# Kernel optimization log

Hardware: AMD Instinct MI355X
Metric: run time of the kernel (lower is better)

Reference implementation:

```python
import jax, jax.numpy as jnp
import numpy as np

D_MODEL, D_STATE, D_CONV, D_INNER, DT_RANK, K = 96, 16, 3, 192, 6, 4
B, H, W = 1, 64, 64


def setup_inputs() -> dict:
    key = jax.random.key(0)
    ks = jax.random.split(key, 10)
    x = jax.random.normal(ks[0], (B, H, W, D_MODEL), jnp.float32)
    in_proj_w = jax.random.normal(ks[1], (2 * D_INNER, D_MODEL), jnp.float32) * 0.02
    conv_w = jax.random.normal(ks[2], (D_INNER, 1, D_CONV, D_CONV), jnp.float32) * 0.1
    conv_b = jnp.zeros((D_INNER,), jnp.float32)
    x_proj_w = jax.random.normal(ks[3], (K, DT_RANK + 2 * D_STATE, D_INNER), jnp.float32) * 0.02
    dt_std = DT_RANK ** -0.5
    dt_w = jax.random.uniform(ks[4], (K, D_INNER, DT_RANK), jnp.float32, -dt_std, dt_std)
    # dt bias init: inv-softplus of dt ~ logUniform(1e-3, 1e-1)
    u = jax.random.uniform(ks[5], (K, D_INNER), jnp.float32)
    dt = jnp.exp(u * (np.log(0.1) - np.log(0.001)) + np.log(0.001)).clip(1e-4)
    dt_b = dt + jnp.log(-jnp.expm1(-dt))
    A_logs = jnp.log(jnp.broadcast_to(jnp.arange(1, D_STATE + 1, dtype=jnp.float32), (K * D_INNER, D_STATE)))
    Ds = jnp.ones((K * D_INNER,), jnp.float32)
    ln_g = jnp.ones((D_INNER,), jnp.float32)
    ln_b = jnp.zeros((D_INNER,), jnp.float32)
    out_proj_w = jax.random.normal(ks[6], (D_MODEL, D_INNER), jnp.float32) * 0.02
    return dict(x=x, in_proj_w=in_proj_w, conv_w=conv_w, conv_b=conv_b, x_proj_w=x_proj_w,
                dt_w=dt_w, dt_b=dt_b, A_logs=A_logs, Ds=Ds, ln_g=ln_g, ln_b=ln_b,
                out_proj_w=out_proj_w)


def _ss2d(x, in_proj_w, conv_w, conv_b, x_proj_w, dt_w, dt_b, A_logs, Ds, ln_g, ln_b, out_proj_w):
    b, h, w, c = x.shape
    L = h * w
    d = conv_w.shape[0]            # d_inner
    n = A_logs.shape[1]            # d_state
    r = dt_w.shape[2]              # dt_rank
    # in_proj + split
    xz = jnp.einsum('bhwc,ec->bhwe', x, in_proj_w)
    xx, z = xz[..., :d], xz[..., d:]
    # depthwise conv (NCHW) + SiLU
    xc = xx.transpose(0, 3, 1, 2)
    pad = (D_CONV - 1) // 2
    xc = jax.lax.conv_general_dilated(xc, conv_w, (1, 1), [(pad, pad), (pad, pad)],
                                      feature_group_count=d) + conv_b[None, :, None, None]
    xc = jax.nn.silu(xc)
    # 4 scan directions: HW, WH, and their reverses
    x_hw = xc.reshape(b, d, L)
    x_wh = xc.transpose(0, 1, 3, 2).reshape(b, d, L)
    xs = jnp.stack([x_hw, x_wh, x_hw[..., ::-1], x_wh[..., ::-1]], axis=1)  # (b,K,d,L)
    x_dbl = jnp.einsum('bkdl,kcd->bkcl', xs, x_proj_w)
    dts, Bs, Cs = x_dbl[:, :, :r], x_dbl[:, :, r:r + n], x_dbl[:, :, r + n:]
    dts = jnp.einsum('bkrl,kdr->bkdl', dts, dt_w)
    delta = jax.nn.softplus(dts + dt_b[None, :, :, None])        # (b,K,d,L)
    A = -jnp.exp(A_logs).reshape(K, d, n)
    # time-major scanned inputs
    dA = jnp.exp(jnp.einsum('bkdl,kdn->lbkdn', delta, A))        # (L,b,K,d,n)
    dBu = jnp.einsum('bkdl,bknl,bkdl->lbkdn', delta, Bs, xs)
    Ct = Cs.transpose(3, 0, 1, 2)                                # (L,b,K,n)
    def step(hst, inp):
        dA_t, dBu_t, C_t = inp
        hst = dA_t * hst + dBu_t
        return hst, jnp.einsum('bkdn,bkn->bkd', hst, C_t)
    h0 = jnp.zeros((b, K, d, n), jnp.float32)
    _, ys = jax.lax.scan(step, h0, (dA, dBu, Ct))                # ys: (L,b,K,d)
    out_y = ys.transpose(1, 2, 3, 0) + xs * Ds.reshape(K, d)[None, :, :, None]
    # recombine directions
    inv = out_y[:, 2:4][..., ::-1]
    y1 = out_y[:, 0]
    y2 = inv[:, 0]
    wh = out_y[:, 1].reshape(b, d, w, h).transpose(0, 1, 3, 2).reshape(b, d, L)
    invwh = inv[:, 1].reshape(b, d, w, h).transpose(0, 1, 3, 2).reshape(b, d, L)
    y = (y1 + y2 + wh + invwh).transpose(0, 2, 1).reshape(b, h, w, d)
    # LayerNorm (eps=1e-5, torch default)
    mu = y.mean(-1, keepdims=True)
    var = ((y - mu) ** 2).mean(-1, keepdims=True)
    y = (y - mu) * jax.lax.rsqrt(var + 1e-5) * ln_g + ln_b
    y = y * jax.nn.silu(z)
    return jnp.einsum('bhwd,cd->bhwc', y, out_proj_w)


def reference(x, in_proj_w, conv_w, conv_b, x_proj_w, dt_w, dt_b, A_logs, Ds, ln_g, ln_b, out_proj_w):
    return _ss2d(x, in_proj_w, conv_w, conv_b, x_proj_w, dt_w, dt_b, A_logs, Ds, ln_g, ln_b, out_proj_w)
```

## Files before the change

### kernel.cpp

```cpp
#include <hip/hip_runtime.h>
#include <hip/hip_bf16.h>

#define LL 4096
#define DM 96
#define DI 192
#define NS 16
#define RK 6
#define RKP 8
#define KD 4
#define CPROJ 38
#define CH 64
#define CS 64
#define NC (KD*DI*NS)
#define PT 32
#define WS 196
#define OT 16
#define L2E 1.44269504f

__device__ __forceinline__ float b2f(__hip_bfloat16 v){ return __bfloat162float(v); }

__device__ __forceinline__ int detect_bf16(const unsigned short* __restrict__ xh, int tid, int* sflag){
  if (tid < 64){
    unsigned short u = xh[2*tid];
    int e = (u >> 7) & 0xFF;
    int sane = (e >= 107 && e <= 131) ? 1 : 0;
    unsigned long long m = __ballot(sane);
    if (tid == 0) *sflag = (__popcll(m) >= 32) ? 1 : 0;
  }
  return 0;
}

struct P12 { const void* p[12]; };
__global__ void k_convert_all(P12 ptrs, float* __restrict__ dst) {
  const int off[13] = {0,393216,430080,431808,432000,461184,465792,466560,
                       478848,479616,479808,480000,498432};
  __shared__ int sflag;
  detect_bf16((const unsigned short*)ptrs.p[0], threadIdx.x, &sflag);
  __syncthreads();
  int f = sflag;
  int i = blockIdx.x * 256 + threadIdx.x;
  if (i >= 498432) return;
  int j = 0;
  #pragma unroll
  for (int s = 1; s < 12; s++) if (i >= off[s]) j = s;
  int e = i - off[j];
  if (f) dst[i] = b2f(((const __hip_bfloat16*)ptrs.p[j])[e]);
  else   dst[i] = ((const float*)ptrs.p[j])[e];
}

__global__ void k_inproj(const float* __restrict__ x,
                         const float* __restrict__ w,
                         float* __restrict__ xx, float* __restrict__ z) {
  __shared__ float xr[8*DM];
  int l0 = blockIdx.x * 8;
  int tid = threadIdx.x;
  for (int i = tid; i < 8*DM; i += 384) xr[i] = x[l0*DM + i];
  __syncthreads();
  int e = tid;
  float acc[8];
  #pragma unroll
  for (int i=0;i<8;i++) acc[i]=0.f;
  const float* wr = w + e*DM;
  for (int c=0;c<DM;c++){
    float wv = wr[c];
    #pragma unroll
    for (int i=0;i<8;i++) acc[i] = fmaf(wv, xr[i*DM+c], acc[i]);
  }
  if (e < DI) {
    #pragma unroll
    for (int i=0;i<8;i++) xx[(l0+i)*DI + e] = acc[i];
  } else {
    int e2 = e - DI;
    #pragma unroll
    for (int i=0;i<8;i++) z[(l0+i)*DI + e2] = acc[i];
  }
}

__global__ void k_conv(const float* __restrict__ xx,
                       const float* __restrict__ cw,
                       const float* __restrict__ cb,
                       float* __restrict__ xc) {
  int l = blockIdx.x;
  int d = threadIdx.x;
  int h = l >> 6, w = l & 63;
  float acc = cb[d];
  #pragma unroll
  for (int ki=0; ki<3; ki++){
    int hh = h + ki - 1;
    if ((unsigned)hh >= 64u) continue;
    #pragma unroll
    for (int kj=0;kj<3;kj++){
      int wj = w + kj - 1;
      if ((unsigned)wj >= 64u) continue;
      acc = fmaf(cw[d*9 + ki*3 + kj], xx[(hh*64+wj)*DI + d], acc);
    }
  }
  xc[l*DI + d] = acc / (1.f + __expf(-acc));
}

__device__ __forceinline__ int dir_map(int k, int t){
  if (k==0) return t;
  if (k==1) return ((t&63)<<6) | (t>>6);
  if (k==2) return 4095 - t;
  int u = 4095 - t; return ((u&63)<<6) | (u>>6);
}

__global__ void __launch_bounds__(256) k_proj(const float* __restrict__ xc,
                       const float* __restrict__ xpw,
                       float* __restrict__ dts,
                       float* __restrict__ Bb, float* __restrict__ Cb) {
  __shared__ float wl[CPROJ*WS];
  __shared__ float xs[PT*WS];
  int b = blockIdx.x;
  int k = b >> 7;
  int t_base = (b & 127) * PT;
  int tid = threadIdx.x;
  for (int idx = tid; idx < CPROJ*DI; idx += 256){
    int cc = idx / DI, j = idx - cc*DI;
    wl[cc*WS + j] = xpw[(k*CPROJ + cc)*DI + j];
  }
  for (int idx = tid; idx < PT*DI; idx += 256){
    int tt = idx / DI, j = idx - tt*DI;
    xs[tt*WS + j] = xc[dir_map(k, t_base + tt)*DI + j];
  }
  __syncthreads();
  int tg = tid & 7;
  int ty = tid >> 3;
  int cc0 = ty;
  int has2 = (ty + 32 < CPROJ);
  int cc1 = has2 ? (ty + 32) : ty;
  float a0x=0.f,a0y=0.f,a0z=0.f,a0w=0.f;
  float a1x=0.f,a1y=0.f,a1z=0.f,a1w=0.f;
  const float4* w0p = (const float4*)&wl[cc0*WS];
  const float4* w1p = (const float4*)&wl[cc1*WS];
  const float4* x0p = (const float4*)&xs[(tg     )*WS];
  const float4* x1p = (const float4*)&xs[(tg +  8)*WS];
  const float4* x2p = (const float4*)&xs[(tg + 16)*WS];
  const float4* x3p = (const float4*)&xs[(tg + 24)*WS];
  #pragma unroll 4
  for (int jc = 0; jc < DI/4; jc++){
    float4 w0 = w0p[jc], w1 = w1p[jc];
    float4 x0 = x0p[jc], x1 = x1p[jc], x2 = x2p[jc], x3 = x3p[jc];
    a0x = fmaf(w0.x,x0.x,fmaf(w0.y,x0.y,fmaf(w0.z,x0.z,fmaf(w0.w,x0.w,a0x))));
    a0y = fmaf(w0.x,x1.x,fmaf(w0.y,x1.y,fmaf(w0.z,x1.z,fmaf(w0.w,x1.w,a0y))));
    a0z = fmaf(w0.x,x2.x,fmaf(w0.y,x2.y,fmaf(w0.z,x2.z,fmaf(w0.w,x2.w,a0z))));
    a0w = fmaf(w0.x,x3.x,fmaf(w0.y,x3.y,fmaf(w0.z,x3.z,fmaf(w0.w,x3.w,a0w))));
    a1x = fmaf(w1.x,x0.x,fmaf(w1.y,x0.y,fmaf(w1.z,x0.z,fmaf(w1.w,x0.w,a1x))));
    a1y = fmaf(w1.x,x1.x,fmaf(w1.y,x1.y,fmaf(w1.z,x1.z,fmaf(w1.w,x1.w,a1y))));
    a1z = fmaf(w1.x,x2.x,fmaf(w1.y,x2.y,fmaf(w1.z,x2.z,fmaf(w1.w,x2.w,a1z))));
    a1w = fmaf(w1.x,x3.x,fmaf(w1.y,x3.y,fmaf(w1.z,x3.z,fmaf(w1.w,x3.w,a1w))));
  }
  float accs0[4] = {a0x,a0y,a0z,a0w};
  float accs1[4] = {a1x,a1y,a1z,a1w};
  #pragma unroll
  for (int i=0;i<4;i++){
    int t = t_base + tg + 8*i;
    size_t kt = (size_t)k*LL + t;
    {
      int cc = cc0; float v = accs0[i];
      if (cc < RK)            dts[kt*RKP + cc] = v;
      else if (cc < RK+NS)    Bb [kt*NS + (cc-RK)] = v;
      else                    Cb [kt*NS + (cc-RK-NS)] = v;
    }
    if (has2){
      int cc = ty + 32; float v = accs1[i];
      if (cc < RK+NS)         Bb [kt*NS + (cc-RK)] = v;
      else                    Cb [kt*NS + (cc-RK-NS)] = v;
    }
  }
}

__global__ void __launch_bounds__(256) k_scan1(
                      const float* __restrict__ xc,
                      const float* __restrict__ dts,
                      const float* __restrict__ Bbuf,
                      const float* __restrict__ A_logs,
                      const float* __restrict__ dtw,
                      const float* __restrict__ dtb,
                      float* __restrict__ Pb, float* __restrict__ Hb) {
  int b = blockIdx.x;
  int k = b / 192;
  int rem = b - k*192;
  int dg3 = rem >> 6, c = rem & 63;
  int tid = threadIdx.x;
  int dl = tid >> 2, nq = tid & 3;
  int d = dg3*64 + dl;
  int kd = k*DI + d;
  float4 Al = *(const float4*)&A_logs[kd*NS + nq*4];
  float A0 = -__expf(Al.x)*L2E, A1 = -__expf(Al.y)*L2E;
  float A2 = -__expf(Al.z)*L2E, A3 = -__expf(Al.w)*L2E;
  float bt = dtb[kd];
  float w0 = dtw[kd*RK+0], w1 = dtw[kd*RK+1], w2 = dtw[kd*RK+2];
  float w3 = dtw[kd*RK+3], w4 = dtw[kd*RK+4], w5 = dtw[kd*RK+5];
  const float* dr = dts + ((size_t)k*LL + c*CS)*RKP;
  const float4* bp = (const float4*)(Bbuf + ((size_t)k*LL + c*CS)*NS) + nq;
  float h0=0.f,h1=0.f,h2=0.f,h3=0.f, P0=1.f,P1=1.f,P2=1.f,P3=1.f;
  for (int s=0; s<CS; s++){
    int t = c*CS + s;
    float4 lo = *(const float4*)(dr + s*RKP);
    float4 hi = *(const float4*)(dr + s*RKP + 4);
    float v = bt;
    v = fmaf(w0, lo.x, v); v = fmaf(w1, lo.y, v); v = fmaf(w2, lo.z, v);
    v = fmaf(w3, lo.w, v); v = fmaf(w4, hi.x, v); v = fmaf(w5, hi.y, v);
    float sp = (v > 20.f) ? v : __logf(1.f + __expf(v));
    float sx = sp * xc[dir_map(k,t)*DI + d];
    float4 bv = bp[s*4];
    float a;
    a = exp2f(sp*A0); h0 = fmaf(a, h0, sx*bv.x); P0 *= a;
    a = exp2f(sp*A1); h1 = fmaf(a, h1, sx*bv.y); P1 *= a;
    a = exp2f(sp*A2); h2 = fmaf(a, h2, sx*bv.z); P2 *= a;
    a = exp2f(sp*A3); h3 = fmaf(a, h3, sx*bv.w); P3 *= a;
  }
  int base = c*NC + kd*NS + nq*4;
  *(float4*)&Pb[base] = make_float4(P0,P1,P2,P3);
  *(float4*)&Hb[base] = make_float4(h0,h1,h2,h3);
}

__global__ void __launch_bounds__(256) k_scan2(
                      const float* __restrict__ Pb, const float* __restrict__ Hb,
                      float* __restrict__ H0) {
  int idx = blockIdx.x*256 + threadIdx.x;
  float h = 0.f;
  #pragma unroll 4
  for (int c=0;c<CH;c++){
    H0[c*NC + idx] = h;
    h = fmaf(Pb[c*NC + idx], h, Hb[c*NC + idx]);
  }
}

__global__ void __launch_bounds__(256) k_scan3(
                      const float* __restrict__ xc,
                      const float* __restrict__ dts,
                      const float* __restrict__ Bbuf,
                      const float* __restrict__ Cbuf,
                      const float* __restrict__ A_logs,
                      const float* __restrict__ dtw,
                      const float* __restrict__ dtb,
                      const float* __restrict__ H0,
                      float* __restrict__ yacc) {
  int b = blockIdx.x;
  int k = b / 192;
  int rem = b - k*192;
  int dg3 = rem >> 6, c = rem & 63;
  int tid = threadIdx.x;
  int dl = tid >> 2, nq = tid & 3;
  int d = dg3*64 + dl;
  int kd = k*DI + d;
  float4 Al = *(const float4*)&A_logs[kd*NS + nq*4];
  float A0 = -__expf(Al.x)*L2E, A1 = -__expf(Al.y)*L2E;
  float A2 = -__expf(Al.z)*L2E, A3 = -__expf(Al.w)*L2E;
  float bt = dtb[kd];
  float w0 = dtw[kd*RK+0], w1 = dtw[kd*RK+1], w2 = dtw[kd*RK+2];
  float w3 = dtw[kd*RK+3], w4 = dtw[kd*RK+4], w5 = dtw[kd*RK+5];
  const float* dr = dts + ((size_t)k*LL + c*CS)*RKP;
  const float4* bp = (const float4*)(Bbuf + ((size_t)k*LL + c*CS)*NS) + nq;
  const float4* cp = (const float4*)(Cbuf + ((size_t)k*LL + c*CS)*NS) + nq;
  float4 hv = *(const float4*)&H0[c*NC + kd*NS + nq*4];
  float h0=hv.x, h1=hv.y, h2=hv.z, h3=hv.w;
  for (int s=0; s<CS; s++){
    int t = c*CS + s;
    float4 lo = *(const float4*)(dr + s*RKP);
    float4 hi = *(const float4*)(dr + s*RKP + 4);
    float v = bt;
    v = fmaf(w0, lo.x, v); v = fmaf(w1, lo.y, v); v = fmaf(w2, lo.z, v);
    v = fmaf(w3, lo.w, v); v = fmaf(w4, hi.x, v); v = fmaf(w5, hi.y, v);
    float sp = (v > 20.f) ? v : __logf(1.f + __expf(v));
    int l = dir_map(k,t);
    float sx = sp * xc[l*DI + d];
    float4 bv = bp[s*4];
    float4 cv = cp[s*4];
    float a;
    a = exp2f(sp*A0); h0 = fmaf(a, h0, sx*bv.x);
    a = exp2f(sp*A1); h1 = fmaf(a, h1, sx*bv.y);
    a = exp2f(sp*A2); h2 = fmaf(a, h2, sx*bv.z);
    a = exp2f(sp*A3); h3 = fmaf(a, h3, sx*bv.w);
    float y = h0*cv.x + h1*cv.y + h2*cv.z + h3*cv.w;
    y += __shfl_xor(y, 1, 64);
    y += __shfl_xor(y, 2, 64);
    if (nq == 0) atomicAdd(&yacc[(size_t)l*DI + d], y);
  }
}

__global__ void k_ln(const float* __restrict__ yacc,
                     const float* __restrict__ xc,
                     const float* __restrict__ z,
                     const float* __restrict__ Ds,
                     const float* __restrict__ ln_g,
                     const float* __restrict__ ln_b,
                     float* __restrict__ g) {
  int l = blockIdx.x;
  int d = threadIdx.x;
  float y = yacc[(size_t)l*DI + d];
  float dsum = Ds[0*DI+d] + Ds[1*DI+d] + Ds[2*DI+d] + Ds[3*DI+d];
  y = fmaf(xc[l*DI+d], dsum, y);
  float s1 = y, s2 = y*y;
  #pragma unroll
  for (int off=32; off; off>>=1){
    s1 += __shfl_xor(s1, off, 64);
    s2 += __shfl_xor(s2, off, 64);
  }
  __shared__ float red[6];
  int wave = d >> 6;
  if ((d & 63) == 0){ red[wave] = s1; red[3+wave] = s2; }
  __syncthreads();
  float sum = red[0]+red[1]+red[2];
  float sq  = red[3]+red[4]+red[5];
  float mu = sum * (1.f/192.f);
  float var = sq * (1.f/192.f) - mu*mu;
  float rstd = rsqrtf(var + 1e-5f);
  float yn = (y - mu) * rstd * ln_g[d] + ln_b[d];
  float zv = z[l*DI + d];
  g[(size_t)l*DI + d] = yn * (zv / (1.f + __expf(-zv)));
}

__global__ void __launch_bounds__(192) k_oproj(const float* __restrict__ g,
                      const float* __restrict__ opw,
                      void* __restrict__ out,
                      const unsigned short* __restrict__ xh) {
  __shared__ float gs[OT*WS];
  __shared__ int sflag;
  int tid = threadIdx.x;
  detect_bf16(xh, tid, &sflag);
  int l0 = blockIdx.x * OT;
  const float4* gsrc = (const float4*)(g + (size_t)l0*DI);
  for (int idx = tid; idx < OT*DI/4; idx += 192){
    int row = idx / 48, col = idx - row*48;
    float4 v = gsrc[idx];
    *(float4*)&gs[row*WS + col*4] = v;
  }
  __syncthreads();
  int half = tid / 96;
  int e = tid - half*96;
  int r0 = half*8;
  float acc[8];
  #pragma unroll
  for (int i=0;i<8;i++) acc[i] = 0.f;
  const float4* wrow = (const float4*)(opw + e*DI);
  #pragma unroll 4
  for (int jc = 0; jc < DI/4; jc++){
    float4 w = wrow[jc];
    #pragma unroll
    for (int i=0;i<8;i++){
      float4 gv = *(const float4*)&gs[(r0+i)*WS + jc*4];
      acc[i] = fmaf(w.x,gv.x,fmaf(w.y,gv.y,fmaf(w.z,gv.z,fmaf(w.w,gv.w,acc[i]))));
    }
  }
  int f = sflag;
  #pragma unroll
  for (int i=0;i<8;i++){
    int l = l0 + r0 + i;
    if (f) ((__hip_bfloat16*)out)[l*DM + e] = __float2bfloat16(acc[i]);
    else   ((float*)out)[l*DM + e] = acc[i];
  }
}

extern "C" void kernel_launch(void* const* d_in, const int* in_sizes, int n_in,
                              void* d_out, int out_size, void* d_ws, size_t ws_size,
                              hipStream_t stream) {
  float* ws = (float*)d_ws;
  float* cvt = ws + 16;
  const int off[13] = {0,393216,430080,431808,432000,461184,465792,466560,
                       478848,479616,479808,480000,498432};
  float* c[12];
  for (int i = 0; i < 12; i++) c[i] = cvt + off[i];

  float* big    = cvt + 498432;
  float* xx     = big;
  float* z      = xx + (size_t)LL*DI;
  float* xc     = z  + (size_t)LL*DI;
  float* dts    = xc + (size_t)LL*DI;
  float* Bb     = dts + (size_t)KD*LL*RKP;
  float* Cb     = Bb + (size_t)KD*LL*NS;
  float* PbYacc = Cb + (size_t)KD*LL*NS;
  float* H0     = PbYacc + (size_t)CH*NC;
  float* Hb     = xx;

  P12 ptrs;
  for (int i = 0; i < 12; i++) ptrs.p[i] = d_in[i];
  k_convert_all<<<(498432 + 255)/256, 256, 0, stream>>>(ptrs, cvt);

  k_inproj<<<LL/8, 384, 0, stream>>>(c[0], c[1], xx, z);
  k_conv<<<LL, DI, 0, stream>>>(xx, c[2], c[3], xc);
  k_proj<<<KD*(LL/PT), 256, 0, stream>>>(xc, c[4], dts, Bb, Cb);
  k_scan1<<<KD*192, 256, 0, stream>>>(xc, dts, Bb, c[7], c[5], c[6], PbYacc, Hb);
  k_scan2<<<NC/256, 256, 0, stream>>>(PbYacc, Hb, H0);
  (void)hipMemsetAsync(PbYacc, 0, (size_t)LL*DI*sizeof(float), stream);
  k_scan3<<<KD*192, 256, 0, stream>>>(xc, dts, Bb, Cb, c[7], c[5], c[6], H0, PbYacc);
  k_ln<<<LL, DI, 0, stream>>>(PbYacc, xc, z, c[8], c[9], c[10], H0);
  k_oproj<<<LL/OT, 192, 0, stream>>>(H0, c[11], d_out, (const unsigned short*)d_in[0]);
}
```

Measured before the change: 223.6 us.

## Make scan chunk count runtime-selectable, using 128 chunks when workspace allows

The chunked selective scan now takes the chunk count as a runtime parameter and picks 128 chunks of 32 steps instead of 64 chunks of 64 steps when the workspace is large enough. This doubles the number of blocks in the two per-chunk scan kernels, shortening each block's serial recurrence and giving the GPU more parallel work. In exchange, the sequential carry-propagation pass runs over twice as many chunks and the prefix state buffers double in size. Buffer aliasing is also reorganized: the carry kernel overwrites the chunk-end states in place, and the output accumulator now reuses the xx buffer.

```diff
diff --git a/kernel.cpp b/kernel.cpp
--- a/kernel.cpp
+++ b/kernel.cpp
@@ -9,8 +9,6 @@
 #define RKP 8
 #define KD 4
 #define CPROJ 38
-#define CH 64
-#define CS 64
 #define NC (KD*DI*NS)
 #define PT 32
 #define WS 196
@@ -177,11 +175,13 @@
                       const float* __restrict__ A_logs,
                       const float* __restrict__ dtw,
                       const float* __restrict__ dtb,
-                      float* __restrict__ Pb, float* __restrict__ Hb) {
+                      float* __restrict__ Pb, float* __restrict__ Hb,
+                      int chBits) {
+  int CSn = LL >> chBits;
   int b = blockIdx.x;
-  int k = b / 192;
-  int rem = b - k*192;
-  int dg3 = rem >> 6, c = rem & 63;
+  int c = b & ((1<<chBits)-1);
+  int kg = b >> chBits;
+  int k = kg / 3, dg3 = kg - k*3;
   int tid = threadIdx.x;
   int dl = tid >> 2, nq = tid & 3;
   int d = dg3*64 + dl;
@@ -192,11 +192,11 @@
   float bt = dtb[kd];
   float w0 = dtw[kd*RK+0], w1 = dtw[kd*RK+1], w2 = dtw[kd*RK+2];
   float w3 = dtw[kd*RK+3], w4 = dtw[kd*RK+4], w5 = dtw[kd*RK+5];
-  const float* dr = dts + ((size_t)k*LL + c*CS)*RKP;
-  const float4* bp = (const float4*)(Bbuf + ((size_t)k*LL + c*CS)*NS) + nq;
+  const float* dr = dts + ((size_t)k*LL + c*CSn)*RKP;
+  const float4* bp = (const float4*)(Bbuf + ((size_t)k*LL + c*CSn)*NS) + nq;
   float h0=0.f,h1=0.f,h2=0.f,h3=0.f, P0=1.f,P1=1.f,P2=1.f,P3=1.f;
-  for (int s=0; s<CS; s++){
-    int t = c*CS + s;
+  for (int s=0; s<CSn; s++){
+    int t = c*CSn + s;
     float4 lo = *(const float4*)(dr + s*RKP);
     float4 hi = *(const float4*)(dr + s*RKP + 4);
     float v = bt;
@@ -217,14 +217,15 @@
 }
 
 __global__ void __launch_bounds__(256) k_scan2(
-                      const float* __restrict__ Pb, const float* __restrict__ Hb,
-                      float* __restrict__ H0) {
+                      const float* __restrict__ Pb, float* __restrict__ Hb,
+                      int CHn) {
   int idx = blockIdx.x*256 + threadIdx.x;
   float h = 0.f;
-  #pragma unroll 4
-  for (int c=0;c<CH;c++){
-    H0[c*NC + idx] = h;
-    h = fmaf(Pb[c*NC + idx], h, Hb[c*NC + idx]);
+  for (int c=0;c<CHn;c++){
+    float P = Pb[c*NC + idx];
+    float Hc = Hb[c*NC + idx];
+    Hb[c*NC + idx] = h;
+    h = fmaf(P, h, Hc);
   }
 }
 
@@ -237,11 +238,13 @@
                       const float* __restrict__ dtw,
                       const float* __restrict__ dtb,
                       const float* __restrict__ H0,
-                      float* __restrict__ yacc) {
+                      float* __restrict__ yacc,
+                      int chBits) {
+  int CSn = LL >> chBits;
   int b = blockIdx.x;
-  int k = b / 192;
-  int rem = b - k*192;
-  int dg3 = rem >> 6, c = rem & 63;
+  int c = b & ((1<<chBits)-1);
+  int kg = b >> chBits;
+  int k = kg / 3, dg3 = kg - k*3;
   int tid = threadIdx.x;
   int dl = tid >> 2, nq = tid & 3;
   int d = dg3*64 + dl;
@@ -252,13 +255,13 @@
   float bt = dtb[kd];
   float w0 = dtw[kd*RK+0], w1 = dtw[kd*RK+1], w2 = dtw[kd*RK+2];
   float w3 = dtw[kd*RK+3], w4 = dtw[kd*RK+4], w5 = dtw[kd*RK+5];
-  const float* dr = dts + ((size_t)k*LL + c*CS)*RKP;
-  const float4* bp = (const float4*)(Bbuf + ((size_t)k*LL + c*CS)*NS) + nq;
-  const float4* cp = (const float4*)(Cbuf + ((size_t)k*LL + c*CS)*NS) + nq;
+  const float* dr = dts + ((size_t)k*LL + c*CSn)*RKP;
+  const float4* bp = (const float4*)(Bbuf + ((size_t)k*LL + c*CSn)*NS) + nq;
+  const float4* cp = (const float4*)(Cbuf + ((size_t)k*LL + c*CSn)*NS) + nq;
   float4 hv = *(const float4*)&H0[c*NC + kd*NS + nq*4];
   float h0=hv.x, h1=hv.y, h2=hv.z, h3=hv.w;
-  for (int s=0; s<CS; s++){
-    int t = c*CS + s;
+  for (int s=0; s<CSn; s++){
+    int t = c*CSn + s;
     float4 lo = *(const float4*)(dr + s*RKP);
     float4 hi = *(const float4*)(dr + s*RKP + 4);
     float v = bt;
@@ -371,9 +374,12 @@
   float* dts    = xc + (size_t)LL*DI;
   float* Bb     = dts + (size_t)KD*LL*RKP;
   float* Cb     = Bb + (size_t)KD*LL*NS;
-  float* PbYacc = Cb + (size_t)KD*LL*NS;
-  float* H0     = PbYacc + (size_t)CH*NC;
-  float* Hb     = xx;
+  float* Pb     = Cb + (size_t)KD*LL*NS;
+  size_t need128 = (size_t)(16 + 498432 + 3*786432 + 131072 + 2*262144 + 2*128*NC) * 4;
+  int chBits = (ws_size >= need128) ? 7 : 6;
+  int CHn = 1 << chBits;
+  float* Hb   = Pb + (size_t)CHn*NC;
+  float* yacc = xx;
 
   P12 ptrs;
   for (int i = 0; i < 12; i++) ptrs.p[i] = d_in[i];
@@ -382,10 +388,10 @@
   k_inproj<<<LL/8, 384, 0, stream>>>(c[0], c[1], xx, z);
   k_conv<<<LL, DI, 0, stream>>>(xx, c[2], c[3], xc);
   k_proj<<<KD*(LL/PT), 256, 0, stream>>>(xc, c[4], dts, Bb, Cb);
-  k_scan1<<<KD*192, 256, 0, stream>>>(xc, dts, Bb, c[7], c[5], c[6], PbYacc, Hb);
-  k_scan2<<<NC/256, 256, 0, stream>>>(PbYacc, Hb, H0);
-  (void)hipMemsetAsync(PbYacc, 0, (size_t)LL*DI*sizeof(float), stream);
-  k_scan3<<<KD*192, 256, 0, stream>>>(xc, dts, Bb, Cb, c[7], c[5], c[6], H0, PbYacc);
-  k_ln<<<LL, DI, 0, stream>>>(PbYacc, xc, z, c[8], c[9], c[10], H0);
-  k_oproj<<<LL/OT, 192, 0, stream>>>(H0, c[11], d_out, (const unsigned short*)d_in[0]);
-}
+  k_scan1<<<KD*3*CHn, 256, 0, stream>>>(xc, dts, Bb, c[7], c[5], c[6], Pb, Hb, chBits);
+  k_scan2<<<NC/256, 256, 0, stream>>>(Pb, Hb, CHn);
+  (void)hipMemsetAsync(yacc, 0, (size_t)LL*DI*sizeof(float), stream);
+  k_scan3<<<KD*3*CHn, 256, 0, stream>>>(xc, dts, Bb, Cb, c[7], c[5], c[6], Hb, yacc, chBits);
+  k_ln<<<LL, DI, 0, stream>>>(yacc, xc, z, c[8], c[9], c[10], Hb);
+  k_oproj<<<LL/OT, 192, 0, stream>>>(Hb, c[11], d_out, (const unsigned short*)d_in[0]);
+}
```

New measurement: 236.5 us. 1.06x slower.
